# Kernel tuning notes

Measured on AMD Instinct MI355X. Metric: run time of the kernel, lower is better.

The kernel has to match this reference:

```python
import jax, jax.numpy as jnp
import numpy as np

WS = 8          # window size M
SHIFT = WS // 2 # cyclic shift
HEADS = 8


def _rel_pos_index(ws):
    # (ws*ws, ws*ws) indices into the (2ws-1)^2 bias table
    coords = np.stack(np.meshgrid(np.arange(ws), np.arange(ws), indexing='ij'), 0).reshape(2, -1)
    rel = coords[:, :, None] - coords[:, None, :]          # (2, N, N)
    rel = rel.transpose(1, 2, 0) + (ws - 1)                # shift to [0, 2ws-2]
    return rel[..., 0] * (2 * ws - 1) + rel[..., 1]        # (N, N)


def _shift_mask(H, W, ws, shift):
    # standard Swin attention mask for shifted windows: (nWin, N, N)
    img = np.zeros((H, W), dtype=np.int32)
    cnt = 0
    for hs in (slice(0, -ws), slice(-ws, -shift), slice(-shift, None)):
        for wsl in (slice(0, -ws), slice(-ws, -shift), slice(-shift, None)):
            img[hs, wsl] = cnt
            cnt += 1
    mw = img.reshape(H // ws, ws, W // ws, ws).transpose(0, 2, 1, 3).reshape(-1, ws * ws)
    diff = mw[:, None, :] - mw[:, :, None]
    return np.where(diff != 0, -100.0, 0.0).astype(np.float32)


def setup_inputs() -> dict:
    key = jax.random.key(0)
    ks = jax.random.split(key, 6)
    B, C, H, W = 32, 256, 64, 64
    return {
        'x': jax.random.normal(ks[0], (B, C, H, W), jnp.float32),
        'w_qkv': jax.random.normal(ks[1], (C, 3 * C), jnp.float32) * (C ** -0.5),
        'b_qkv': jnp.zeros((3 * C,), jnp.float32),
        'w_o': jax.random.normal(ks[2], (C, C), jnp.float32) * (C ** -0.5),
        'b_o': jnp.zeros((C,), jnp.float32),
        'rel_bias_table': jax.random.normal(ks[3], ((2 * WS - 1) ** 2, HEADS), jnp.float32) * 0.02,
    }


def reference(x, w_qkv, b_qkv, w_o, b_o, rel_bias_table):
    B, C, H, W = x.shape
    ws, shift, heads = WS, SHIFT, HEADS
    dh = C // heads
    nH, nW = H // ws, W // ws
    nWin, N = nH * nW, ws * ws

    rel_idx = jnp.asarray(_rel_pos_index(ws))                 # (N, N) int
    mask = jnp.asarray(_shift_mask(H, W, ws, shift))          # (nWin, N, N)

    # cyclic shift
    xs = jnp.roll(x, (-shift, -shift), axis=(2, 3))
    # window partition: (B, C, H, W) -> (B, nWin, N, C)
    xw = xs.reshape(B, C, nH, ws, nW, ws).transpose(0, 2, 4, 3, 5, 1).reshape(B, nWin, N, C)

    qkv = xw @ w_qkv + b_qkv                                  # (B, nWin, N, 3C)
    qkv = qkv.reshape(B, nWin, N, 3, heads, dh)
    q = qkv[..., 0, :, :].transpose(0, 1, 3, 2, 4)            # (B, nWin, h, N, dh)
    k = qkv[..., 1, :, :].transpose(0, 1, 3, 2, 4)
    v = qkv[..., 2, :, :].transpose(0, 1, 3, 2, 4)

    attn = jnp.einsum('bwhnd,bwhmd->bwhnm', q, k) * (dh ** -0.5)
    bias = rel_bias_table[rel_idx]                            # (N, N, heads)
    attn = attn + bias.transpose(2, 0, 1)[None, None]         # add rel pos bias
    attn = attn + mask[None, :, None]                         # add shift mask
    attn = jax.nn.softmax(attn, axis=-1)

    out = jnp.einsum('bwhnm,bwhmd->bwhnd', attn, v)           # (B, nWin, h, N, dh)
    out = out.transpose(0, 1, 3, 2, 4).reshape(B, nWin, N, C)
    out = out @ w_o + b_o

    # window reverse: (B, nWin, N, C) -> (B, C, H, W)
    out = out.reshape(B, nH, nW, ws, ws, C).transpose(0, 5, 1, 3, 2, 4).reshape(B, C, H, W)
    # reverse cyclic shift
    return jnp.roll(out, (shift, shift), axis=(2, 3))
```

## Files before the change

### kernel.cpp

```cpp
#include <hip/hip_runtime.h>
#include <stdint.h>

typedef __attribute__((ext_vector_type(8))) short short8;
typedef __attribute__((ext_vector_type(4))) float floatx4;
typedef unsigned short u16;
typedef unsigned int u32;

#define MFMA16(a,b,c) __builtin_amdgcn_mfma_f32_16x16x32_bf16((a),(b),(c),0,0,0)

__device__ __forceinline__ u16 f2b(float f){
  u32 i; __builtin_memcpy(&i,&f,4); i += 0x7FFFu + ((i>>16)&1u); return (u16)(i>>16);
}
__device__ __forceinline__ int regid(int p){ return (p<56)?0:((p<60)?1:2); }

#define SCO 16896
#define LDS_ELEMS 26112

__global__ void prep_w(const float* __restrict__ wqkv, const float* __restrict__ wo,
                       u16* __restrict__ wqkvT, u16* __restrict__ woT){
  int idx = blockIdx.x*256 + threadIdx.x;
  if(idx < 768*256){ int n = idx>>8, k = idx&255; wqkvT[idx] = f2b(wqkv[k*768 + n]); }
  else { int j = idx - 768*256; int n = j>>8, k = j&255; woT[j] = f2b(wo[k*256 + n]); }
}

__global__ __launch_bounds__(256,3) void swmsa_attn(
    const float* __restrict__ x, const u16* __restrict__ wqkvT, const float* __restrict__ bqkv,
    const float* __restrict__ table, u16* __restrict__ yws)
{
  extern __shared__ u16 lds[];
  const int tid  = threadIdx.x;
  const int wave = tid>>6, lane = tid&63;
  const int quad = lane>>4, colid = lane&15;
  const int bi = blockIdx.x;
  const int xcd = bi & 7, j = bi >> 3;
  const int r0 = ((j >> 3) << 3) | xcd;
  const int wx = j & 7;
  const int b = r0 >> 3, wy = r0 & 7;
  const size_t imgbase = (size_t)b*256*4096;
  const int w0 = wx*8+4;
  const floatx4 fzero = {0.f,0.f,0.f,0.f};
  u16* sc = lds + SCO + wave*2304;

  for(int i=0;i<2;++i){
    int unit = tid + 256*i;
    int cg = unit>>3, ty = unit&7;
    int hs = (wy*8+ty+4)&63;
    u16 vv[4][8];
    #pragma unroll
    for(int cc=0;cc<4;++cc){
      const float* src = x + imgbase + (size_t)(cg*4+cc)*4096 + (size_t)hs*64;
      floatx4 lo, hi;
      if(wx<7){ lo = *(const floatx4*)(src+w0); hi = *(const floatx4*)(src+w0+4); }
      else    { lo = *(const floatx4*)(src+60); hi = *(const floatx4*)(src); }
      #pragma unroll
      for(int t=0;t<4;++t){ vv[cc][t]=f2b(lo[t]); vv[cc][4+t]=f2b(hi[t]); }
    }
    #pragma unroll
    for(int t=0;t<8;++t){
      uint64_t pk = (uint64_t)vv[0][t] | ((uint64_t)vv[1][t]<<16)
                  | ((uint64_t)vv[2][t]<<32) | ((uint64_t)vv[3][t]<<48);
      *(uint64_t*)&lds[(ty*8+t)*264 + cg*4] = pk;
    }
  }
  __syncthreads();

  short8 aq2[2][4], bk2[2][4], bv2[2][2][2];
  for(int t3=0; t3<3; ++t3){
    const int cc = 2 - t3;
    const int col0 = (cc*4 + wave)*64;
    const u16* wslab = wqkvT + (size_t)(col0+colid)*256 + quad*8;
    floatx4 acc[4][4];
    #pragma unroll
    for(int mt=0;mt<4;++mt)
      #pragma unroll
      for(int nt=0;nt<4;++nt) acc[mt][nt] = fzero;
    short8 bcur[4], bnxt[4];
    #pragma unroll
    for(int nt=0;nt<4;++nt) bcur[nt] = *(const short8*)&wslab[(size_t)nt*16*256];
    for(int k0=0;k0<256;k0+=32){
      short8 af[4];
      #pragma unroll
      for(int mt=0;mt<4;++mt) af[mt]  = *(const short8*)&lds[(mt*16+colid)*264 + k0 + quad*8];
      if(k0 < 224){
        #pragma unroll
        for(int nt=0;nt<4;++nt) bnxt[nt] = *(const short8*)&wslab[(size_t)nt*16*256 + k0 + 32];
      }
      #pragma unroll
      for(int mt=0;mt<4;++mt)
        #pragma unroll
        for(int nt=0;nt<4;++nt) acc[mt][nt] = MFMA16(af[mt], bcur[nt], acc[mt][nt]);
      #pragma unroll
      for(int nt=0;nt<4;++nt) bcur[nt] = bnxt[nt];
    }
    #pragma unroll
    for(int hf=0; hf<2; ++hf){
      #pragma unroll
      for(int nt2=0; nt2<2; ++nt2){
        int nt = hf*2 + nt2;
        float bias = bqkv[col0 + nt*16 + colid];
        #pragma unroll
        for(int mt=0;mt<4;++mt)
          #pragma unroll
          for(int rr=0;rr<4;++rr){
            int row = mt*16 + quad*4 + rr;
            u16 bvv = f2b(acc[mt][nt][rr] + bias);
            if(cc==2) sc[(nt2*16+colid)*72 + row] = bvv;
            else      sc[row*36 + nt2*16 + colid] = bvv;
          }
      }
      if(cc==2){
        #pragma unroll
        for(int n2=0;n2<2;++n2)
          #pragma unroll
          for(int kc=0;kc<2;++kc)
            bv2[hf][n2][kc] = *(const short8*)&sc[(n2*16+colid)*72 + kc*32 + quad*8];
      } else if(cc==1){
        #pragma unroll
        for(int mt=0;mt<4;++mt) bk2[hf][mt] = *(const short8*)&sc[(mt*16+colid)*36 + quad*8];
      } else {
        #pragma unroll
        for(int mt=0;mt<4;++mt) aq2[hf][mt] = *(const short8*)&sc[(mt*16+colid)*36 + quad*8];
      }
    }
  }
  __syncthreads();

  const float scale = 0.17677669529663687f;
  #pragma unroll
  for(int hi=0; hi<2; ++hi){
    const int h = wave*2 + hi;
    floatx4 s[4][4];
    #pragma unroll
    for(int mt=0;mt<4;++mt)
      #pragma unroll
      for(int nt=0;nt<4;++nt) s[mt][nt] = MFMA16(aq2[hi][mt], bk2[hi][nt], fzero);
    int cntk[4], kys[4], kxs[4];
    #pragma unroll
    for(int nt=0;nt<4;++nt){
      int col = nt*16 + colid;
      kys[nt] = col>>3; kxs[nt] = col&7;
      cntk[nt] = regid(wy*8 + kys[nt])*3 + regid(wx*8 + kxs[nt]);
    }
    #pragma unroll
    for(int mt=0;mt<4;++mt)
      #pragma unroll
      for(int rr=0;rr<4;++rr){
        int row = mt*16 + quad*4 + rr;
        int ty = row>>3, tx = row&7;
        int cntq = regid(wy*8+ty)*3 + regid(wx*8+tx);
        #pragma unroll
        for(int nt=0;nt<4;++nt){
          int rel = (ty - kys[nt] + 7)*15 + (tx - kxs[nt] + 7);
          float add = table[rel*8 + h] + ((cntq==cntk[nt]) ? 0.f : -100.f);
          s[mt][nt][rr] = s[mt][nt][rr]*scale + add;
        }
      }
    u32 gpk[4][4];
    #pragma unroll
    for(int mt=0;mt<4;++mt)
      #pragma unroll
      for(int rr=0;rr<4;++rr){
        float mx = s[mt][0][rr];
        #pragma unroll
        for(int nt=1;nt<4;++nt) mx = fmaxf(mx, s[mt][nt][rr]);
        #pragma unroll
        for(int d=1; d<16; d<<=1) mx = fmaxf(mx, __shfl_xor(mx, d));
        float e[4], sum = 0.f;
        #pragma unroll
        for(int nt=0;nt<4;++nt){ e[nt] = __expf(s[mt][nt][rr]-mx); sum += e[nt]; }
        #pragma unroll
        for(int d=1; d<16; d<<=1) sum += __shfl_xor(sum, d);
        float inv = 1.0f/sum;
        int row = mt*16 + quad*4 + rr;
        sc[row*36 + colid]      = f2b(e[0]*inv);
        sc[row*36 + 16 + colid] = f2b(e[1]*inv);
        gpk[mt][rr] = (u32)f2b(e[2]*inv) | ((u32)f2b(e[3]*inv) << 16);
      }
    floatx4 o[4][2];
    #pragma unroll
    for(int mt=0;mt<4;++mt){ o[mt][0]=fzero; o[mt][1]=fzero; }
    #pragma unroll
    for(int kc=0;kc<2;++kc){
      if(kc==1){
        #pragma unroll
        for(int mt=0;mt<4;++mt)
          #pragma unroll
          for(int rr=0;rr<4;++rr){
            int row = mt*16 + quad*4 + rr;
            sc[row*36 + colid]      = (u16)(gpk[mt][rr] & 0xffffu);
            sc[row*36 + 16 + colid] = (u16)(gpk[mt][rr] >> 16);
          }
      }
      short8 ap[4];
      #pragma unroll
      for(int mt=0;mt<4;++mt) ap[mt] = *(const short8*)&sc[(mt*16+colid)*36 + quad*8];
      #pragma unroll
      for(int mt=0;mt<4;++mt)
        #pragma unroll
        for(int n2=0;n2<2;++n2) o[mt][n2] = MFMA16(ap[mt], bv2[hi][n2][kc], o[mt][n2]);
    }
    #pragma unroll
    for(int n2=0;n2<2;++n2){
      int c = h*32 + n2*16 + colid;
      #pragma unroll
      for(int mt=0;mt<4;++mt)
        #pragma unroll
        for(int rr=0;rr<4;++rr)
          lds[(mt*16+quad*4+rr)*264 + c] = f2b(o[mt][n2][rr]);
    }
  }
  __syncthreads();

  const size_t bandbase = (size_t)r0 * (512*256);
  #pragma unroll
  for(int i=0;i<8;++i){
    int unit = i*256 + tid;
    int tokw = unit>>5, c8 = unit&31;
    int tyw = tokw>>3, txw = tokw&7;
    int cg = (8*wx + 4 + txw) & 63;
    size_t t = (size_t)(tyw*64 + cg);
    *(short8*)&yws[bandbase + t*256 + c8*8] = *(const short8*)&lds[tokw*264 + c8*8];
  }
}

__global__ __launch_bounds__(256,2) void swmsa_proj(
    const u16* __restrict__ yws, const u16* __restrict__ woT,
    const float* __restrict__ bo, float* __restrict__ out)
{
  const int tid = threadIdx.x;
  const int wave = tid>>6, lane = tid&63;
  const int quad = lane>>4, colid = lane&15;
  const int bi = blockIdx.x;
  const int xcd = bi&7, jj = bi>>3;
  const int band = ((jj>>4)<<3) | xcd;
  const int sub = jj&15, q4 = sub>>2, npp = sub&3;
  const int b = band>>3, wy = band&7;
  const u16* ybase = yws + (size_t)band*(512*256) + (size_t)q4*(128*256);
  const int ch = npp*64 + wave*16 + colid;
  const u16* wbase = woT + (size_t)ch*256 + quad*8;
  const u16* abase = ybase + (size_t)colid*256 + quad*8;
  const floatx4 fz = {0.f,0.f,0.f,0.f};
  floatx4 acc[8];
  #pragma unroll
  for(int mt=0;mt<8;++mt) acc[mt]=fz;

  #pragma unroll
  for(int kk=0;kk<8;++kk){
    short8 bw = *(const short8*)&wbase[kk*32];
    #pragma unroll
    for(int mt=0;mt<8;++mt){
      short8 a = *(const short8*)&abase[(size_t)mt*16*256 + kk*32];
      acc[mt] = MFMA16(a, bw, acc[mt]);
    }
  }

  const float bias = bo[ch];
  float* obase = out + (size_t)b*256*4096 + (size_t)ch*4096;
  #pragma unroll
  for(int mt=0;mt<8;++mt){
    int ty = mt>>2;
    int hd = (wy*8 + q4*2 + ty + 4) & 63;
    int colb = (mt&3)*16 + quad*4;
    floatx4 v = acc[mt];
    v[0]+=bias; v[1]+=bias; v[2]+=bias; v[3]+=bias;
    *(floatx4*)(obase + (size_t)hd*64 + colb) = v;
  }
}

__global__ __launch_bounds__(256,3) void swmsa_fused(
    const float* __restrict__ x, const u16* __restrict__ wqkvT, const float* __restrict__ bqkv,
    const u16* __restrict__ woT, const float* __restrict__ bo, const float* __restrict__ table,
    float* __restrict__ out)
{
  extern __shared__ u16 lds[];
  const int tid  = threadIdx.x;
  const int wave = tid>>6, lane = tid&63;
  const int quad = lane>>4, colid = lane&15;
  const int bi = blockIdx.x;
  const int xcd = bi & 7, j = bi >> 3;
  const int r0 = ((j >> 3) << 3) | xcd;
  const int wx = j & 7;
  const int b = r0 >> 3, wy = r0 & 7;
  const size_t imgbase = (size_t)b*256*4096;
  const int w0 = wx*8+4;
  const floatx4 fzero = {0.f,0.f,0.f,0.f};
  u16* sc = lds + SCO + wave*2304;

  for(int i=0;i<2;++i){
    int unit = tid + 256*i;
    int cg = unit>>3, ty = unit&7;
    int hs = (wy*8+ty+4)&63;
    u16 vv[4][8];
    #pragma unroll
    for(int cc=0;cc<4;++cc){
      const float* src = x + imgbase + (size_t)(cg*4+cc)*4096 + (size_t)hs*64;
      floatx4 lo, hi;
      if(wx<7){ lo = *(const floatx4*)(src+w0); hi = *(const floatx4*)(src+w0+4); }
      else    { lo = *(const floatx4*)(src+60); hi = *(const floatx4*)(src); }
      #pragma unroll
      for(int t=0;t<4;++t){ vv[cc][t]=f2b(lo[t]); vv[cc][4+t]=f2b(hi[t]); }
    }
    #pragma unroll
    for(int t=0;t<8;++t){
      uint64_t pk = (uint64_t)vv[0][t] | ((uint64_t)vv[1][t]<<16)
                  | ((uint64_t)vv[2][t]<<32) | ((uint64_t)vv[3][t]<<48);
      *(uint64_t*)&lds[(ty*8+t)*264 + cg*4] = pk;
    }
  }
  __syncthreads();

  short8 aq2[2][4], bk2[2][4], bv2[2][2][2];
  for(int t3=0; t3<3; ++t3){
    const int cc = 2 - t3;
    const int col0 = (cc*4 + wave)*64;
    const u16* wslab = wqkvT + (size_t)(col0+colid)*256 + quad*8;
    floatx4 acc[4][4];
    #pragma unroll
    for(int mt=0;mt<4;++mt)
      #pragma unroll
      for(int nt=0;nt<4;++nt) acc[mt][nt] = fzero;
    short8 bcur[4], bnxt[4];
    #pragma unroll
    for(int nt=0;nt<4;++nt) bcur[nt] = *(const short8*)&wslab[(size_t)nt*16*256];
    for(int k0=0;k0<256;k0+=32){
      short8 af[4];
      #pragma unroll
      for(int mt=0;mt<4;++mt) af[mt]  = *(const short8*)&lds[(mt*16+colid)*264 + k0 + quad*8];
      if(k0 < 224){
        #pragma unroll
        for(int nt=0;nt<4;++nt) bnxt[nt] = *(const short8*)&wslab[(size_t)nt*16*256 + k0 + 32];
      }
      #pragma unroll
      for(int mt=0;mt<4;++mt)
        #pragma unroll
        for(int nt=0;nt<4;++nt) acc[mt][nt] = MFMA16(af[mt], bcur[nt], acc[mt][nt]);
      #pragma unroll
      for(int nt=0;nt<4;++nt) bcur[nt] = bnxt[nt];
    }
    #pragma unroll
    for(int hf=0; hf<2; ++hf){
      #pragma unroll
      for(int nt2=0; nt2<2; ++nt2){
        int nt = hf*2 + nt2;
        float bias = bqkv[col0 + nt*16 + colid];
        #pragma unroll
        for(int mt=0;mt<4;++mt)
          #pragma unroll
          for(int rr=0;rr<4;++rr){
            int row = mt*16 + quad*4 + rr;
            u16 bvv = f2b(acc[mt][nt][rr] + bias);
            if(cc==2) sc[(nt2*16+colid)*72 + row] = bvv;
            else      sc[row*36 + nt2*16 + colid] = bvv;
          }
      }
      if(cc==2){
        #pragma unroll
        for(int n2=0;n2<2;++n2)
          #pragma unroll
          for(int kc=0;kc<2;++kc)
            bv2[hf][n2][kc] = *(const short8*)&sc[(n2*16+colid)*72 + kc*32 + quad*8];
      } else if(cc==1){
        #pragma unroll
        for(int mt=0;mt<4;++mt) bk2[hf][mt] = *(const short8*)&sc[(mt*16+colid)*36 + quad*8];
      } else {
        #pragma unroll
        for(int mt=0;mt<4;++mt) aq2[hf][mt] = *(const short8*)&sc[(mt*16+colid)*36 + quad*8];
      }
    }
  }
  __syncthreads();

  const float scale = 0.17677669529663687f;
  #pragma unroll
  for(int hi=0; hi<2; ++hi){
    const int h = wave*2 + hi;
    floatx4 s[4][4];
    #pragma unroll
    for(int mt=0;mt<4;++mt)
      #pragma unroll
      for(int nt=0;nt<4;++nt) s[mt][nt] = MFMA16(aq2[hi][mt], bk2[hi][nt], fzero);
    int cntk[4], kys[4], kxs[4];
    #pragma unroll
    for(int nt=0;nt<4;++nt){
      int col = nt*16 + colid;
      kys[nt] = col>>3; kxs[nt] = col&7;
      cntk[nt] = regid(wy*8 + kys[nt])*3 + regid(wx*8 + kxs[nt]);
    }
    #pragma unroll
    for(int mt=0;mt<4;++mt)
      #pragma unroll
      for(int rr=0;rr<4;++rr){
        int row = mt*16 + quad*4 + rr;
        int ty = row>>3, tx = row&7;
        int cntq = regid(wy*8+ty)*3 + regid(wx*8+tx);
        #pragma unroll
        for(int nt=0;nt<4;++nt){
          int rel = (ty - kys[nt] + 7)*15 + (tx - kxs[nt] + 7);
          float add = table[rel*8 + h] + ((cntq==cntk[nt]) ? 0.f : -100.f);
          s[mt][nt][rr] = s[mt][nt][rr]*scale + add;
        }
      }
    u32 gpk[4][4];
    #pragma unroll
    for(int mt=0;mt<4;++mt)
      #pragma unroll
      for(int rr=0;rr<4;++rr){
        float mx = s[mt][0][rr];
        #pragma unroll
        for(int nt=1;nt<4;++nt) mx = fmaxf(mx, s[mt][nt][rr]);
        #pragma unroll
        for(int d=1; d<16; d<<=1) mx = fmaxf(mx, __shfl_xor(mx, d));
        float e[4], sum = 0.f;
        #pragma unroll
        for(int nt=0;nt<4;++nt){ e[nt] = __expf(s[mt][nt][rr]-mx); sum += e[nt]; }
        #pragma unroll
        for(int d=1; d<16; d<<=1) sum += __shfl_xor(sum, d);
        float inv = 1.0f/sum;
        int row = mt*16 + quad*4 + rr;
        sc[row*36 + colid]      = f2b(e[0]*inv);
        sc[row*36 + 16 + colid] = f2b(e[1]*inv);
        gpk[mt][rr] = (u32)f2b(e[2]*inv) | ((u32)f2b(e[3]*inv) << 16);
      }
    floatx4 o[4][2];
    #pragma unroll
    for(int mt=0;mt<4;++mt){ o[mt][0]=fzero; o[mt][1]=fzero; }
    #pragma unroll
    for(int kc=0;kc<2;++kc){
      if(kc==1){
        #pragma unroll
        for(int mt=0;mt<4;++mt)
          #pragma unroll
          for(int rr=0;rr<4;++rr){
            int row = mt*16 + quad*4 + rr;
            sc[row*36 + colid]      = (u16)(gpk[mt][rr] & 0xffffu);
            sc[row*36 + 16 + colid] = (u16)(gpk[mt][rr] >> 16);
          }
      }
      short8 ap[4];
      #pragma unroll
      for(int mt=0;mt<4;++mt) ap[mt] = *(const short8*)&sc[(mt*16+colid)*36 + quad*8];
      #pragma unroll
      for(int mt=0;mt<4;++mt)
        #pragma unroll
        for(int n2=0;n2<2;++n2) o[mt][n2] = MFMA16(ap[mt], bv2[hi][n2][kc], o[mt][n2]);
    }
    #pragma unroll
    for(int n2=0;n2<2;++n2){
      int c = h*32 + n2*16 + colid;
      #pragma unroll
      for(int mt=0;mt<4;++mt)
        #pragma unroll
        for(int rr=0;rr<4;++rr)
          lds[(mt*16+quad*4+rr)*264 + c] = f2b(o[mt][n2][rr]);
    }
  }
  __syncthreads();

  {
    floatx4 acc[4][4];
    #pragma unroll
    for(int np=0;np<4;++np)
      #pragma unroll
      for(int mt=0;mt<4;++mt) acc[np][mt] = fzero;
    const u16* wbase = woT + (size_t)(wave*16+colid)*256 + quad*8;
    for(int k0=0;k0<256;k0+=32){
      short8 ay[4];
      #pragma unroll
      for(int mt=0;mt<4;++mt) ay[mt] = *(const short8*)&lds[(mt*16+colid)*264 + k0 + quad*8];
      #pragma unroll
      for(int np=0;np<4;++np){
        short8 bw = *(const short8*)&wbase[(size_t)np*16384 + k0];
        #pragma unroll
        for(int mt=0;mt<4;++mt) acc[np][mt] = MFMA16(ay[mt], bw, acc[np][mt]);
      }
    }
    const int ty_base = quad>>1, txg = quad&1;
    const int col = (wx<7) ? (w0 + 4*txg) : (txg ? 0 : 60);
    #pragma unroll
    for(int np=0;np<4;++np){
      const int ch = np*64 + wave*16 + colid;
      const float bias = bo[ch];
      float* chbase = out + imgbase + (size_t)ch*4096;
      #pragma unroll
      for(int mt=0;mt<4;++mt){
        int ty = 2*mt + ty_base;
        int hd = (wy*8 + ty + 4)&63;
        floatx4 vsto = acc[np][mt];
        vsto[0]+=bias; vsto[1]+=bias; vsto[2]+=bias; vsto[3]+=bias;
        *(floatx4*)(chbase + (size_t)hd*64 + col) = vsto;
      }
    }
  }
}

extern "C" void kernel_launch(void* const* d_in, const int* in_sizes, int n_in,
                              void* d_out, int out_size, void* d_ws, size_t ws_size,
                              hipStream_t stream) {
  const float* x     = (const float*)d_in[0];
  const float* wqkv  = (const float*)d_in[1];
  const float* bqkv  = (const float*)d_in[2];
  const float* wo    = (const float*)d_in[3];
  const float* bo    = (const float*)d_in[4];
  const float* table = (const float*)d_in[5];
  float* out = (float*)d_out;

  u16* wqkvT = (u16*)d_ws;
  u16* woT   = wqkvT + 768*256;
  u16* yws   = woT   + 256*256;

  const size_t need = (size_t)(768*256 + 256*256)*2 + (size_t)256*512*256*2;

  prep_w<<<1024, 256, 0, stream>>>(wqkv, wo, wqkvT, woT);

  if(ws_size >= need){
    (void)hipFuncSetAttribute((const void*)swmsa_attn,
                              hipFuncAttributeMaxDynamicSharedMemorySize, LDS_ELEMS*2);
    swmsa_attn<<<2048, 256, LDS_ELEMS*2, stream>>>(x, wqkvT, bqkv, table, yws);
    swmsa_proj<<<4096, 256, 0, stream>>>(yws, woT, bo, out);
  } else {
    (void)hipFuncSetAttribute((const void*)swmsa_fused,
                              hipFuncAttributeMaxDynamicSharedMemorySize, LDS_ELEMS*2);
    swmsa_fused<<<2048, 256, LDS_ELEMS*2, stream>>>(x, wqkvT, bqkv, woT, bo, table, out);
  }
}
```

Measured before the change: 559.3 us.

## Store attention output and Wo in MFMA fragment-tiled layout for projection

The attention kernel now writes its bf16 output in a tiled layout that matches the MFMA fragments, and a new prep kernel builds the Wo transpose in the same layout. The projection kernel then reads each A/B fragment from one contiguous 1KB chunk per wave instead of 16 rows strided by 512 bytes, giving fully coalesced loads. Occupancy for the projection kernel goes up to 4 blocks per CU. This adds a small extra prep launch and workspace.

```diff
diff --git a/kernel.cpp b/kernel.cpp
--- a/kernel.cpp
+++ b/kernel.cpp
@@ -21,6 +21,13 @@
   int idx = blockIdx.x*256 + threadIdx.x;
   if(idx < 768*256){ int n = idx>>8, k = idx&255; wqkvT[idx] = f2b(wqkv[k*768 + n]); }
   else { int j = idx - 768*256; int n = j>>8, k = j&255; woT[j] = f2b(wo[k*256 + n]); }
+}
+
+__global__ void prep_wf(const float* __restrict__ wo, u16* __restrict__ woTf){
+  int idx = blockIdx.x*256 + threadIdx.x;
+  int n = idx>>8, k = idx&255;
+  int cht = n>>4, cl = n&15, kk = k>>5, q = (k>>3)&3, e = k&7;
+  woTf[(size_t)(cht*8+kk)*512 + cl*32 + q*8 + e] = f2b(wo[k*256 + n]);
 }
 
 __global__ __launch_bounds__(256,3) void swmsa_attn(
@@ -211,20 +218,22 @@
   }
   __syncthreads();
 
-  const size_t bandbase = (size_t)r0 * (512*256);
+  const size_t bandbase = (size_t)r0 * 131072;
   #pragma unroll
   for(int i=0;i<8;++i){
     int unit = i*256 + tid;
     int tokw = unit>>5, c8 = unit&31;
     int tyw = tokw>>3, txw = tokw&7;
     int cg = (8*wx + 4 + txw) & 63;
-    size_t t = (size_t)(tyw*64 + cg);
-    *(short8*)&yws[bandbase + t*256 + c8*8] = *(const short8*)&lds[tokw*264 + c8*8];
-  }
-}
-
-__global__ __launch_bounds__(256,2) void swmsa_proj(
-    const u16* __restrict__ yws, const u16* __restrict__ woT,
+    int t = tyw*64 + cg;
+    int kk = c8>>2, q = c8&3;
+    size_t dst = bandbase + (size_t)((t>>4)*8 + kk)*512 + (t&15)*32 + q*8;
+    *(short8*)&yws[dst] = *(const short8*)&lds[tokw*264 + c8*8];
+  }
+}
+
+__global__ __launch_bounds__(256,4) void swmsa_proj(
+    const u16* __restrict__ yfrag, const u16* __restrict__ woTf,
     const float* __restrict__ bo, float* __restrict__ out)
 {
   const int tid = threadIdx.x;
@@ -235,10 +244,9 @@
   const int band = ((jj>>4)<<3) | xcd;
   const int sub = jj&15, q4 = sub>>2, npp = sub&3;
   const int b = band>>3, wy = band&7;
-  const u16* ybase = yws + (size_t)band*(512*256) + (size_t)q4*(128*256);
-  const int ch = npp*64 + wave*16 + colid;
-  const u16* wbase = woT + (size_t)ch*256 + quad*8;
-  const u16* abase = ybase + (size_t)colid*256 + quad*8;
+  const int cht = npp*4 + wave;
+  const u16* abase = yfrag + (size_t)band*131072 + (size_t)(q4*8)*8*512 + colid*32 + quad*8;
+  const u16* bbase = woTf + (size_t)(cht*8)*512 + colid*32 + quad*8;
   const floatx4 fz = {0.f,0.f,0.f,0.f};
   floatx4 acc[8];
   #pragma unroll
@@ -246,14 +254,15 @@
 
   #pragma unroll
   for(int kk=0;kk<8;++kk){
-    short8 bw = *(const short8*)&wbase[kk*32];
+    short8 bw = *(const short8*)&bbase[kk*512];
     #pragma unroll
     for(int mt=0;mt<8;++mt){
-      short8 a = *(const short8*)&abase[(size_t)mt*16*256 + kk*32];
+      short8 a = *(const short8*)&abase[(size_t)(mt*8+kk)*512];
       acc[mt] = MFMA16(a, bw, acc[mt]);
     }
   }
 
+  const int ch = cht*16 + colid;
   const float bias = bo[ch];
   float* obase = out + (size_t)b*256*4096 + (size_t)ch*4096;
   #pragma unroll
@@ -506,17 +515,19 @@
 
   u16* wqkvT = (u16*)d_ws;
   u16* woT   = wqkvT + 768*256;
-  u16* yws   = woT   + 256*256;
-
-  const size_t need = (size_t)(768*256 + 256*256)*2 + (size_t)256*512*256*2;
+  u16* woTf  = woT   + 256*256;
+  u16* yws   = woTf  + 256*256;
+
+  const size_t need = (size_t)(768*256 + 256*256 + 256*256)*2 + (size_t)256*512*256*2;
 
   prep_w<<<1024, 256, 0, stream>>>(wqkv, wo, wqkvT, woT);
 
   if(ws_size >= need){
+    prep_wf<<<256, 256, 0, stream>>>(wo, woTf);
     (void)hipFuncSetAttribute((const void*)swmsa_attn,
                               hipFuncAttributeMaxDynamicSharedMemorySize, LDS_ELEMS*2);
     swmsa_attn<<<2048, 256, LDS_ELEMS*2, stream>>>(x, wqkvT, bqkv, table, yws);
-    swmsa_proj<<<4096, 256, 0, stream>>>(yws, woT, bo, out);
+    swmsa_proj<<<4096, 256, 0, stream>>>(yws, woTf, bo, out);
   } else {
     (void)hipFuncSetAttribute((const void*)swmsa_fused,
                               hipFuncAttributeMaxDynamicSharedMemorySize, LDS_ELEMS*2);
```

Measured after the change: 516.4 us. -7.7%, faster.
